# Performance work log

Hardware: AMD Instinct MI355X
Metric: run time of the kernel (lower is better)

The kernel has to match this reference:

```python
import jax, jax.numpy as jnp
import numpy as np

N, E = 50000, 400000
EMB, IN, HID, HEADS = 128, 128, 128, 3
RRELU_SLOPE = (1.0 / 8.0 + 1.0 / 3.0) / 2.0  # torch.rrelu eval-mode slope


def _gat_conv(h_in, src, dst, W, a_src, a_dst, b, concat):
    """PyG-style GATConv. h_in: [N, F_in]; src/dst: [E'] (self-loops included)."""
    n = h_in.shape[0]
    h = (h_in @ W).reshape(n, HEADS, -1)            # [N, H, C]
    e_src = jnp.sum(h * a_src, axis=-1)             # [N, H]
    e_dst = jnp.sum(h * a_dst, axis=-1)             # [N, H]
    e = jax.nn.leaky_relu(e_src[src] + e_dst[dst], 0.2)  # [E', H]
    # softmax over incoming edges of each target node
    m = jax.ops.segment_max(e, dst, num_segments=n)
    ex = jnp.exp(e - m[dst])
    denom = jax.ops.segment_sum(ex, dst, num_segments=n)
    alpha = ex / denom[dst]                          # [E', H]
    out = jax.ops.segment_sum(h[src] * alpha[:, :, None], dst, num_segments=n)  # [N,H,C]
    out = out.reshape(n, -1) if concat else out.mean(axis=1)
    return out + b


def _rrelu(x):
    return jnp.where(x >= 0, x, x * RRELU_SLOPE)


def setup_inputs() -> dict:
    key = jax.random.key(0)
    ks = jax.random.split(key, 16)
    d_in = IN + EMB

    def glorot(k, shape):
        fan = sum(shape)
        return jax.random.normal(k, shape, jnp.float32) * np.sqrt(2.0 / fan)

    return {
        "z": jax.random.normal(ks[0], (N, EMB), jnp.float32),
        "x": jax.random.normal(ks[1], (N, IN), jnp.float32),
        "ei": jax.random.randint(ks[2], (2, E), 0, N, jnp.int32),
        "W1": glorot(ks[3], (d_in, HEADS * HID)),
        "a1_src": glorot(ks[4], (HEADS, HID)),
        "a1_dst": glorot(ks[5], (HEADS, HID)),
        "b1": jnp.zeros((HID,), jnp.float32),                 # concat=False -> size C
        "W2": glorot(ks[6], (HID, HEADS * HID)),
        "a2_src": glorot(ks[7], (HEADS, HID)),
        "a2_dst": glorot(ks[8], (HEADS, HID)),
        "b2": jnp.zeros((HEADS * HID,), jnp.float32),         # concat=True -> size H*C
        "W_lin": glorot(ks[9], (HEADS * HID, 1)),
        "b_lin": jnp.zeros((1,), jnp.float32),
    }


def reference(z, x, ei, W1, a1_src, a1_dst, b1, W2, a2_src, a2_dst, b2, W_lin, b_lin):
    n = x.shape[0]
    loops = jnp.arange(n, dtype=ei.dtype)
    src = jnp.concatenate([ei[0], loops])  # PyG add_self_loops=True
    dst = jnp.concatenate([ei[1], loops])
    h = jnp.concatenate([z, x], axis=1)
    h = _rrelu(_gat_conv(h, src, dst, W1, a1_src, a1_dst, b1, concat=False))
    h = _rrelu(_gat_conv(h, src, dst, W2, a2_src, a2_dst, b2, concat=True))
    return jax.nn.sigmoid(h @ W_lin + b_lin)
```

## Files before the change

### kernel.cpp

```cpp
#include <hip/hip_runtime.h>
#include <stdint.h>

#define HEADS 3
#define HID 128
#define FDIM (HEADS * HID)

typedef __attribute__((ext_vector_type(8))) short bf16x8;
typedef __attribute__((ext_vector_type(4))) float f32x4;

__device__ __forceinline__ float lrelu(float x) { return x >= 0.f ? x : 0.2f * x; }
__device__ __forceinline__ float rrelu(float x) {
    const float SLOPE = (1.0f / 8.0f + 1.0f / 3.0f) * 0.5f;
    return x >= 0.f ? x : SLOPE * x;
}
__device__ __forceinline__ unsigned short f2bf(float f) {
    union { float f; unsigned u; } c; c.f = f;
    unsigned r = c.u + 0x7FFF + ((c.u >> 16) & 1);
    return (unsigned short)(r >> 16);
}
__device__ __forceinline__ float bflo(unsigned u) {
    union { unsigned u; float f; } c; c.u = u << 16; return c.f;
}
__device__ __forceinline__ float bfhi(unsigned u) {
    union { unsigned u; float f; } c; c.u = u & 0xffff0000u; return c.f;
}

__device__ __forceinline__ void gload_lds16(const void* g, void* l) {
    __builtin_amdgcn_global_load_lds(
        (const __attribute__((address_space(1))) void*)g,
        (__attribute__((address_space(3))) void*)l, 16, 0, 0);
}


__global__ void k_hist(const int* __restrict__ dst, int E, int* __restrict__ cnt) {
    for (int i = blockIdx.x * blockDim.x + threadIdx.x; i < E; i += gridDim.x * blockDim.x)
        atomicAdd(&cnt[dst[i]], 1);
}

#define SC_T 256
#define SC_E 8
#define SC_CHUNK (SC_T * SC_E)

__global__ __launch_bounds__(SC_T) void k_scan1(const int* __restrict__ cnt,
                                                int* __restrict__ exc,
                                                int* __restrict__ bsum, int n) {
    __shared__ int sm[SC_T];
    int b = blockIdx.x, t = threadIdx.x;
    int base = b * SC_CHUNK + t * SC_E;
    int v[SC_E];
    int s = 0;
#pragma unroll
    for (int i = 0; i < SC_E; i++) {
        int idx = base + i;
        v[i] = (idx < n) ? cnt[idx] : 0;
        s += v[i];
    }
    sm[t] = s;
    __syncthreads();
    for (int off = 1; off < SC_T; off <<= 1) {
        int x = (t >= off) ? sm[t - off] : 0;
        __syncthreads();
        sm[t] += x;
        __syncthreads();
    }
    int run = sm[t] - s;
    if (t == SC_T - 1) bsum[b] = sm[t];
#pragma unroll
    for (int i = 0; i < SC_E; i++) {
        int idx = base + i;
        if (idx < n) exc[idx] = run;
        run += v[i];
    }
}

__global__ __launch_bounds__(256) void k_scan2(const int* __restrict__ bsum,
                                               int* __restrict__ bpre, int nb) {
    __shared__ int sm[256];
    int t = threadIdx.x;
    int v = (t < nb) ? bsum[t] : 0;
    sm[t] = v;
    __syncthreads();
    for (int off = 1; off < 256; off <<= 1) {
        int x = (t >= off) ? sm[t - off] : 0;
        __syncthreads();
        sm[t] += x;
        __syncthreads();
    }
    if (t < nb) bpre[t + 1] = sm[t];
    if (t == 0) bpre[0] = 0;
}

__global__ void k_scan3(int* __restrict__ offs, const int* __restrict__ bpre,
                        int* __restrict__ cursor, int n, int nb) {
    int i = blockIdx.x * blockDim.x + threadIdx.x;
    if (i < n) {
        int o = offs[i] + bpre[i / SC_CHUNK];
        offs[i] = o;
        cursor[i] = o;
    }
    if (i == 0) offs[n] = bpre[nb];
}

__global__ void k_scatter(const int* __restrict__ src, const int* __restrict__ dst, int E,
                          int* __restrict__ cursor, int* __restrict__ ssrc,
                          int* __restrict__ sdst) {
    for (int i = blockIdx.x * blockDim.x + threadIdx.x; i < E; i += gridDim.x * blockDim.x) {
        int d = dst[i];
        int p = atomicAdd(&cursor[d], 1);
        ssrc[p] = src[i];
        sdst[p] = d;
    }
}


__global__ void k_cvt_concat(const float* __restrict__ z, const float* __restrict__ x,
                             unsigned short* __restrict__ A, int Nn, int Mpad) {
    int total = Mpad * 64;
    for (int i = blockIdx.x * blockDim.x + threadIdx.x; i < total;
         i += gridDim.x * blockDim.x) {
        int row = i >> 6;
        int c4 = (i & 63) * 4;
        float4 v = make_float4(0.f, 0.f, 0.f, 0.f);
        if (row < Nn) {
            const float* sp = (c4 < 128) ? (z + (size_t)row * 128 + c4)
                                         : (x + (size_t)row * 128 + (c4 - 128));
            v = *(const float4*)sp;
        }
        unsigned short o[4] = {f2bf(v.x), f2bf(v.y), f2bf(v.z), f2bf(v.w)};
        *(uint2*)&A[(size_t)row * 256 + c4] = *(uint2*)o;
    }
}

__global__ void k_cvt_wt(const float* __restrict__ W, unsigned short* __restrict__ WT,
                         int K, int Ncols) {
    int n = blockIdx.x;
    for (int k = threadIdx.x; k < K; k += blockDim.x)
        WT[(size_t)n * K + k] = f2bf(W[(size_t)k * Ncols + n]);
}


__global__ __launch_bounds__(256) void k_gemm_bf16(
    const unsigned short* __restrict__ A,
    const unsigned short* __restrict__ BT,
    unsigned short* __restrict__ C,
    int K, int Ncols,
    const float* __restrict__ asrc, const float* __restrict__ adst,
    float* __restrict__ es, float* __restrict__ ed, int Nnodes) {
    __shared__ __align__(16) unsigned short As[128 * 32];
    __shared__ __align__(16) unsigned short Bs[128 * 32];
    __shared__ float esP[128][2], edP[128][2];
    int tid = threadIdx.x;
    int w = tid >> 6, lane = tid & 63;
    int row0 = blockIdx.x * 128;
    int col0 = blockIdx.y * 128;
    int wr = w >> 1, wc = w & 1;

    f32x4 acc[4][4] = {};
    int frow = lane & 15;
    int fk = (lane >> 4) * 8;

    for (int k0 = 0; k0 < K; k0 += 32) {
#pragma unroll
        for (int i = 0; i < 2; i++) {
            int c = (i * 4 + w) * 64 + lane;
            gload_lds16(A + (size_t)(row0 + (c >> 2)) * K + k0 + (c & 3) * 8,
                        (char*)As + (i * 4 + w) * 1024);
        }
#pragma unroll
        for (int i = 0; i < 2; i++) {
            int c = (i * 4 + w) * 64 + lane;
            gload_lds16(BT + (size_t)(col0 + (c >> 2)) * K + k0 + (c & 3) * 8,
                        (char*)Bs + (i * 4 + w) * 1024);
        }
        asm volatile("s_waitcnt vmcnt(0)" ::: "memory");
        __syncthreads();

        bf16x8 af[4], bfr[4];
#pragma unroll
        for (int m = 0; m < 4; m++)
            af[m] = *(const bf16x8*)&As[(wr * 64 + m * 16 + frow) * 32 + fk];
#pragma unroll
        for (int n = 0; n < 4; n++)
            bfr[n] = *(const bf16x8*)&Bs[(wc * 64 + n * 16 + frow) * 32 + fk];
#pragma unroll
        for (int m = 0; m < 4; m++)
#pragma unroll
            for (int n = 0; n < 4; n++)
                acc[m][n] = __builtin_amdgcn_mfma_f32_16x16x32_bf16(af[m], bfr[n], acc[m][n], 0, 0, 0);
        __syncthreads();
    }

    int ccol = lane & 15, crow = (lane >> 4) * 4;

#pragma unroll
    for (int m = 0; m < 4; m++)
#pragma unroll
        for (int n = 0; n < 4; n++)
#pragma unroll
            for (int j = 0; j < 4; j++) {
                int r = row0 + wr * 64 + m * 16 + crow + j;
                int cc = col0 + wc * 64 + n * 16 + ccol;
                C[(size_t)r * Ncols + cc] = f2bf(acc[m][n][j]);
            }

    int head = blockIdx.y;
    float as4[4], ad4[4];
#pragma unroll
    for (int n = 0; n < 4; n++) {
        int col_sub = wc * 64 + n * 16 + ccol;
        as4[n] = asrc[head * HID + col_sub];
        ad4[n] = adst[head * HID + col_sub];
    }
#pragma unroll
    for (int m = 0; m < 4; m++)
#pragma unroll
        for (int j = 0; j < 4; j++) {
            float ps = 0.f, pd = 0.f;
#pragma unroll
            for (int n = 0; n < 4; n++) {
                float v = acc[m][n][j];
                ps = fmaf(v, as4[n], ps);
                pd = fmaf(v, ad4[n], pd);
            }
#pragma unroll
            for (int off = 1; off < 16; off <<= 1) {
                ps += __shfl_xor(ps, off);
                pd += __shfl_xor(pd, off);
            }
            if (ccol == 0) {
                int row_sub = wr * 64 + m * 16 + crow + j;
                esP[row_sub][wc] = ps;
                edP[row_sub][wc] = pd;
            }
        }
    __syncthreads();
    if (tid < 128) {
        int r = row0 + tid;
        if (r < Nnodes) {
            es[(size_t)r * 3 + head] = esP[tid][0] + esP[tid][1];
            ed[(size_t)r * 3 + head] = edP[tid][0] + edP[tid][1];
        }
    }
}


__global__ void k_edge_w(const int* __restrict__ ssrc, const int* __restrict__ sdst,
                         const float* __restrict__ es, const float* __restrict__ ed,
                         float4* __restrict__ w4, int E) {
    for (int j = blockIdx.x * blockDim.x + threadIdx.x; j < E; j += gridDim.x * blockDim.x) {
        int s = ssrc[j], d = sdst[j];
        float w0 = __expf(lrelu(es[s * 3 + 0] + ed[d * 3 + 0]));
        float w1 = __expf(lrelu(es[s * 3 + 1] + ed[d * 3 + 1]));
        float w2 = __expf(lrelu(es[s * 3 + 2] + ed[d * 3 + 2]));
        w4[j] = make_float4(w0, w1, w2, 0.f);
    }
}

__global__ void k_den(const float* __restrict__ es, const float* __restrict__ ed,
                      const int* __restrict__ offs, const float4* __restrict__ w4,
                      float4* __restrict__ wself, float4* __restrict__ invden, int Nn) {
    for (int n = blockIdx.x * blockDim.x + threadIdx.x; n < Nn; n += gridDim.x * blockDim.x) {
        float s0 = __expf(lrelu(es[n * 3 + 0] + ed[n * 3 + 0]));
        float s1 = __expf(lrelu(es[n * 3 + 1] + ed[n * 3 + 1]));
        float s2 = __expf(lrelu(es[n * 3 + 2] + ed[n * 3 + 2]));
        float d0 = s0, d1 = s1, d2 = s2;
        int j0 = offs[n], j1 = offs[n + 1];
        int j = j0;
        for (; j + 4 <= j1; j += 4) {
            float4 a = w4[j], b = w4[j + 1], c = w4[j + 2], d = w4[j + 3];
            d0 += a.x + b.x + c.x + d.x;
            d1 += a.y + b.y + c.y + d.y;
            d2 += a.z + b.z + c.z + d.z;
        }
        for (; j < j1; j++) {
            float4 w = w4[j];
            d0 += w.x; d1 += w.y; d2 += w.z;
        }
        wself[n] = make_float4(s0, s1, s2, 0.f);
        invden[n] = make_float4(1.f / d0, 1.f / d1, 1.f / d2, 0.f);
    }
}


#define EDGE_UNROLL4(body)                                                       \
    int j = j0;                                                                  \
    for (; j + 4 <= j1; j += 4) {                                                \
        int si[4]; float4 wv[4]; unsigned uu[4][3];                              \
        _Pragma("unroll") for (int e = 0; e < 4; e++) si[e] = ssrc[j + e];       \
        _Pragma("unroll") for (int e = 0; e < 4; e++) wv[e] = w4[j + e];         \
        _Pragma("unroll") for (int e = 0; e < 4; e++) {                          \
            const unsigned* rp = Hu + (size_t)si[e] * 192 + L;                   \
            uu[e][0] = rp[0]; uu[e][1] = rp[64]; uu[e][2] = rp[128];             \
        }                                                                        \
        _Pragma("unroll") for (int e = 0; e < 4; e++) { body(wv[e], uu[e]) }     \
    }                                                                            \
    for (; j < j1; j++) {                                                        \
        int s1_ = ssrc[j]; float4 w_ = w4[j];                                    \
        const unsigned* rp = Hu + (size_t)s1_ * 192 + L;                         \
        unsigned u_[3] = {rp[0], rp[64], rp[128]};                               \
        { body(w_, u_) }                                                         \
    }

#define ACC3(wv, uv)                                                             \
    a0[0] = fmaf(wv.x, bflo(uv[0]), a0[0]); a1[0] = fmaf(wv.x, bfhi(uv[0]), a1[0]); \
    a0[1] = fmaf(wv.y, bflo(uv[1]), a0[1]); a1[1] = fmaf(wv.y, bfhi(uv[1]), a1[1]); \
    a0[2] = fmaf(wv.z, bflo(uv[2]), a0[2]); a1[2] = fmaf(wv.z, bfhi(uv[2]), a1[2]);

__global__ __launch_bounds__(256) void k_agg_mean(const unsigned* __restrict__ Hu,
                                                  const float4* __restrict__ w4,
                                                  const float4* __restrict__ wself,
                                                  const float4* __restrict__ invden,
                                                  const int* __restrict__ offs,
                                                  const int* __restrict__ ssrc,
                                                  const float* __restrict__ b,
                                                  unsigned* __restrict__ out, int Nn) {
    int L = threadIdx.x & 63;
    int wstep = gridDim.x * 4;
    for (int n = blockIdx.x * 4 + (threadIdx.x >> 6); n < Nn; n += wstep) {
        float4 ws = wself[n];
        const unsigned* rp = Hu + (size_t)n * 192 + L;
        unsigned u0 = rp[0], u1 = rp[64], u2 = rp[128];
        float a0[3] = {ws.x * bflo(u0), ws.y * bflo(u1), ws.z * bflo(u2)};
        float a1[3] = {ws.x * bfhi(u0), ws.y * bfhi(u1), ws.z * bfhi(u2)};
        int j0 = offs[n], j1 = offs[n + 1];
        EDGE_UNROLL4(ACC3)
        float4 iv = invden[n];
        int c0 = 2 * L;
        float2 bb = *(const float2*)&b[c0];
        float m0 = (a0[0] * iv.x + a0[1] * iv.y + a0[2] * iv.z) * (1.f / 3.f) + bb.x;
        float m1 = (a1[0] * iv.x + a1[1] * iv.y + a1[2] * iv.z) * (1.f / 3.f) + bb.y;
        unsigned short o[2] = {f2bf(rrelu(m0)), f2bf(rrelu(m1))};
        out[(size_t)n * 64 + L] = *(unsigned*)o;
    }
}

__global__ __launch_bounds__(256) void k_agg_cat_final(const unsigned* __restrict__ Hu,
                                                       const float4* __restrict__ w4,
                                                       const float4* __restrict__ wself,
                                                       const float4* __restrict__ invden,
                                                       const int* __restrict__ offs,
                                                       const int* __restrict__ ssrc,
                                                       const float* __restrict__ b,
                                                       const float* __restrict__ Wl,
                                                       const float* __restrict__ bl,
                                                       float* __restrict__ out, int Nn) {
    int L = threadIdx.x & 63;
    int wstep = gridDim.x * 4;
    for (int n = blockIdx.x * 4 + (threadIdx.x >> 6); n < Nn; n += wstep) {
        float4 ws = wself[n];
        const unsigned* rp = Hu + (size_t)n * 192 + L;
        unsigned u0 = rp[0], u1 = rp[64], u2 = rp[128];
        float a0[3] = {ws.x * bflo(u0), ws.y * bflo(u1), ws.z * bflo(u2)};
        float a1[3] = {ws.x * bfhi(u0), ws.y * bfhi(u1), ws.z * bfhi(u2)};
        int j0 = offs[n], j1 = offs[n + 1];
        EDGE_UNROLL4(ACC3)
        float4 iv = invden[n];
        float ivv[3] = {iv.x, iv.y, iv.z};
        float p = 0.f;
#pragma unroll
        for (int k = 0; k < 3; k++) {
            int col = k * HID + 2 * L;
            float2 bb = *(const float2*)&b[col];
            float2 wl = *(const float2*)&Wl[col];
            float r0 = rrelu(a0[k] * ivv[k] + bb.x);
            float r1 = rrelu(a1[k] * ivv[k] + bb.y);
            p = fmaf(r0, wl.x, p);
            p = fmaf(r1, wl.y, p);
        }
#pragma unroll
        for (int off = 32; off > 0; off >>= 1) p += __shfl_down(p, off);
        if (L == 0) out[n] = 1.f / (1.f + __expf(-(p + bl[0])));
    }
}


extern "C" void kernel_launch(void* const* d_in, const int* in_sizes, int n_in,
                              void* d_out, int out_size, void* d_ws, size_t ws_size,
                              hipStream_t stream) {
    const float* z   = (const float*)d_in[0];
    const float* x   = (const float*)d_in[1];
    const int*   ei  = (const int*)d_in[2];
    const float* W1  = (const float*)d_in[3];
    const float* a1s = (const float*)d_in[4];
    const float* a1d = (const float*)d_in[5];
    const float* b1  = (const float*)d_in[6];
    const float* W2  = (const float*)d_in[7];
    const float* a2s = (const float*)d_in[8];
    const float* a2d = (const float*)d_in[9];
    const float* b2  = (const float*)d_in[10];
    const float* Wl  = (const float*)d_in[11];
    const float* bl  = (const float*)d_in[12];
    float* outp = (float*)d_out;

    int Nn = in_sizes[0] / 128;
    int E  = in_sizes[2] / 2;
    int Mpad = (Nn + 127) & ~127;
    int nb = (Nn + SC_CHUNK - 1) / SC_CHUNK;

    char* p = (char*)d_ws;
    auto carve = [&](size_t bytes) -> char* {
        char* r = p;
        p += (bytes + 255) & ~(size_t)255;
        return r;
    };
    int*            offs   = (int*)carve((size_t)(Nn + 1) * 4);
    int*            cursor = (int*)carve((size_t)Nn * 4);
    int*            ssrc   = (int*)carve((size_t)E * 4);
    int*            sdst   = (int*)carve((size_t)E * 4);
    int*            bsum   = (int*)carve((size_t)(nb + 1) * 4);
    int*            bpre   = (int*)carve((size_t)(nb + 1) * 4);
    float*          e1s    = (float*)carve((size_t)Nn * 3 * 4);
    float*          e1d    = (float*)carve((size_t)Nn * 3 * 4);
    float4*         w4     = (float4*)carve((size_t)E * 16);
    float4*         wself  = (float4*)carve((size_t)Nn * 16);
    float4*         invden = (float4*)carve((size_t)Nn * 16);
    unsigned short* Abf    = (unsigned short*)carve((size_t)Mpad * 256 * 2);
    unsigned short* W1T    = (unsigned short*)carve((size_t)FDIM * 256 * 2);
    unsigned short* W2T    = (unsigned short*)carve((size_t)FDIM * 128 * 2);
    unsigned short* Hbf    = (unsigned short*)carve((size_t)Mpad * FDIM * 2);
    unsigned short* H2in   = (unsigned short*)carve((size_t)Mpad * 128 * 2);

    const int* srcI = ei;
    const int* dstI = ei + E;

    hipMemsetAsync(cursor, 0, (size_t)Nn * 4, stream);
    k_hist<<<256, 256, 0, stream>>>(dstI, E, cursor);
    k_scan1<<<nb, SC_T, 0, stream>>>(cursor, offs, bsum, Nn);
    k_scan2<<<1, 256, 0, stream>>>(bsum, bpre, nb);
    k_scan3<<<(Nn + 255) / 256, 256, 0, stream>>>(offs, bpre, cursor, Nn, nb);
    k_scatter<<<256, 256, 0, stream>>>(srcI, dstI, E, cursor, ssrc, sdst);

    k_cvt_concat<<<2048, 256, 0, stream>>>(z, x, Abf, Nn, Mpad);
    k_cvt_wt<<<FDIM, 256, 0, stream>>>(W1, W1T, 256, FDIM);
    k_cvt_wt<<<FDIM, 128, 0, stream>>>(W2, W2T, 128, FDIM);
    hipMemsetAsync(H2in + (size_t)Nn * 128, 0, (size_t)(Mpad - Nn) * 128 * 2, stream);

    dim3 gg(Mpad / 128, FDIM / 128);

    k_gemm_bf16<<<gg, 256, 0, stream>>>(Abf, W1T, Hbf, 256, FDIM, a1s, a1d, e1s, e1d, Nn);
    k_edge_w<<<1024, 256, 0, stream>>>(ssrc, sdst, e1s, e1d, w4, E);
    k_den<<<(Nn + 255) / 256, 256, 0, stream>>>(e1s, e1d, offs, w4, wself, invden, Nn);
    k_agg_mean<<<2048, 256, 0, stream>>>((const unsigned*)Hbf, w4, wself, invden, offs,
                                         ssrc, b1, (unsigned*)H2in, Nn);

    k_gemm_bf16<<<gg, 256, 0, stream>>>(H2in, W2T, Hbf, 128, FDIM, a2s, a2d, e1s, e1d, Nn);
    k_edge_w<<<1024, 256, 0, stream>>>(ssrc, sdst, e1s, e1d, w4, E);
    k_den<<<(Nn + 255) / 256, 256, 0, stream>>>(e1s, e1d, offs, w4, wself, invden, Nn);
    k_agg_cat_final<<<2048, 256, 0, stream>>>((const unsigned*)Hbf, w4, wself, invden, offs,
                                              ssrc, b2, Wl, bl, outp, Nn);
}
```

Before: 266.7 us.

## Fuse fp32-to-bf16 conversion into GEMM and softmax denominator into aggregation

The first GEMM now reads z and x as fp32 directly, converting to bf16 while staging into LDS, which removes the separate concat/convert kernel and its intermediate buffer. The per-node denominator kernel is dropped: the aggregation kernels compute the self-loop weight and accumulate the softmax denominator alongside the weighted feature sum. Grid sizes for histogram and scatter are raised. In exchange, the A tile is loaded through registers instead of direct-to-LDS, which may stall the GEMM, and every lane redundantly sums the denominator.

```diff
diff --git a/kernel.cpp b/kernel.cpp
--- a/kernel.cpp
+++ b/kernel.cpp
@@ -113,24 +113,6 @@
 }
 
 
-__global__ void k_cvt_concat(const float* __restrict__ z, const float* __restrict__ x,
-                             unsigned short* __restrict__ A, int Nn, int Mpad) {
-    int total = Mpad * 64;
-    for (int i = blockIdx.x * blockDim.x + threadIdx.x; i < total;
-         i += gridDim.x * blockDim.x) {
-        int row = i >> 6;
-        int c4 = (i & 63) * 4;
-        float4 v = make_float4(0.f, 0.f, 0.f, 0.f);
-        if (row < Nn) {
-            const float* sp = (c4 < 128) ? (z + (size_t)row * 128 + c4)
-                                         : (x + (size_t)row * 128 + (c4 - 128));
-            v = *(const float4*)sp;
-        }
-        unsigned short o[4] = {f2bf(v.x), f2bf(v.y), f2bf(v.z), f2bf(v.w)};
-        *(uint2*)&A[(size_t)row * 256 + c4] = *(uint2*)o;
-    }
-}
-
 __global__ void k_cvt_wt(const float* __restrict__ W, unsigned short* __restrict__ WT,
                          int K, int Ncols) {
     int n = blockIdx.x;
@@ -139,8 +121,9 @@
 }
 
 
-__global__ __launch_bounds__(256) void k_gemm_bf16(
-    const unsigned short* __restrict__ A,
+template <bool F32A>
+__global__ __launch_bounds__(256) void k_gemm(
+    const void* __restrict__ Ap0, const void* __restrict__ Ap1, int Nn,
     const unsigned short* __restrict__ BT,
     unsigned short* __restrict__ C,
     int K, int Ncols,
@@ -160,17 +143,49 @@
     int fk = (lane >> 4) * 8;
 
     for (int k0 = 0; k0 < K; k0 += 32) {
-#pragma unroll
-        for (int i = 0; i < 2; i++) {
-            int c = (i * 4 + w) * 64 + lane;
-            gload_lds16(A + (size_t)(row0 + (c >> 2)) * K + k0 + (c & 3) * 8,
-                        (char*)As + (i * 4 + w) * 1024);
-        }
-#pragma unroll
-        for (int i = 0; i < 2; i++) {
-            int c = (i * 4 + w) * 64 + lane;
-            gload_lds16(BT + (size_t)(col0 + (c >> 2)) * K + k0 + (c & 3) * 8,
-                        (char*)Bs + (i * 4 + w) * 1024);
+        if (F32A) {
+            const float* zf = (const float*)Ap0;
+            const float* xf = (const float*)Ap1;
+            float4 va[4];
+#pragma unroll
+            for (int i = 0; i < 4; i++) {
+                int idx = i * 256 + tid;
+                int row = idx >> 3;
+                int c4 = (idx & 7) * 4;
+                int gr = row0 + row;
+                const float* sp = (k0 < 128)
+                                      ? (zf + (size_t)gr * 128 + k0 + c4)
+                                      : (xf + (size_t)gr * 128 + (k0 - 128) + c4);
+                va[i] = (gr < Nn) ? *(const float4*)sp
+                                  : make_float4(0.f, 0.f, 0.f, 0.f);
+            }
+#pragma unroll
+            for (int i = 0; i < 2; i++) {
+                int c = (i * 4 + w) * 64 + lane;
+                gload_lds16(BT + (size_t)(col0 + (c >> 2)) * K + k0 + (c & 3) * 8,
+                            (char*)Bs + (i * 4 + w) * 1024);
+            }
+#pragma unroll
+            for (int i = 0; i < 4; i++) {
+                int idx = i * 256 + tid;
+                unsigned short o[4] = {f2bf(va[i].x), f2bf(va[i].y),
+                                       f2bf(va[i].z), f2bf(va[i].w)};
+                *(uint2*)((char*)As + (size_t)idx * 8) = *(uint2*)o;
+            }
+        } else {
+            const unsigned short* A = (const unsigned short*)Ap0;
+#pragma unroll
+            for (int i = 0; i < 2; i++) {
+                int c = (i * 4 + w) * 64 + lane;
+                gload_lds16(A + (size_t)(row0 + (c >> 2)) * K + k0 + (c & 3) * 8,
+                            (char*)As + (i * 4 + w) * 1024);
+            }
+#pragma unroll
+            for (int i = 0; i < 2; i++) {
+                int c = (i * 4 + w) * 64 + lane;
+                gload_lds16(BT + (size_t)(col0 + (c >> 2)) * K + k0 + (c & 3) * 8,
+                            (char*)Bs + (i * 4 + w) * 1024);
+            }
         }
         asm volatile("s_waitcnt vmcnt(0)" ::: "memory");
         __syncthreads();
@@ -253,31 +268,6 @@
         float w1 = __expf(lrelu(es[s * 3 + 1] + ed[d * 3 + 1]));
         float w2 = __expf(lrelu(es[s * 3 + 2] + ed[d * 3 + 2]));
         w4[j] = make_float4(w0, w1, w2, 0.f);
-    }
-}
-
-__global__ void k_den(const float* __restrict__ es, const float* __restrict__ ed,
-                      const int* __restrict__ offs, const float4* __restrict__ w4,
-                      float4* __restrict__ wself, float4* __restrict__ invden, int Nn) {
-    for (int n = blockIdx.x * blockDim.x + threadIdx.x; n < Nn; n += gridDim.x * blockDim.x) {
-        float s0 = __expf(lrelu(es[n * 3 + 0] + ed[n * 3 + 0]));
-        float s1 = __expf(lrelu(es[n * 3 + 1] + ed[n * 3 + 1]));
-        float s2 = __expf(lrelu(es[n * 3 + 2] + ed[n * 3 + 2]));
-        float d0 = s0, d1 = s1, d2 = s2;
-        int j0 = offs[n], j1 = offs[n + 1];
-        int j = j0;
-        for (; j + 4 <= j1; j += 4) {
-            float4 a = w4[j], b = w4[j + 1], c = w4[j + 2], d = w4[j + 3];
-            d0 += a.x + b.x + c.x + d.x;
-            d1 += a.y + b.y + c.y + d.y;
-            d2 += a.z + b.z + c.z + d.z;
-        }
-        for (; j < j1; j++) {
-            float4 w = w4[j];
-            d0 += w.x; d1 += w.y; d2 += w.z;
-        }
-        wself[n] = make_float4(s0, s1, s2, 0.f);
-        invden[n] = make_float4(1.f / d0, 1.f / d1, 1.f / d2, 0.f);
     }
 }
 
@@ -304,12 +294,13 @@
 #define ACC3(wv, uv)                                                             \
     a0[0] = fmaf(wv.x, bflo(uv[0]), a0[0]); a1[0] = fmaf(wv.x, bfhi(uv[0]), a1[0]); \
     a0[1] = fmaf(wv.y, bflo(uv[1]), a0[1]); a1[1] = fmaf(wv.y, bfhi(uv[1]), a1[1]); \
-    a0[2] = fmaf(wv.z, bflo(uv[2]), a0[2]); a1[2] = fmaf(wv.z, bfhi(uv[2]), a1[2]);
+    a0[2] = fmaf(wv.z, bflo(uv[2]), a0[2]); a1[2] = fmaf(wv.z, bfhi(uv[2]), a1[2]); \
+    den0 += wv.x; den1 += wv.y; den2 += wv.z;
 
 __global__ __launch_bounds__(256) void k_agg_mean(const unsigned* __restrict__ Hu,
                                                   const float4* __restrict__ w4,
-                                                  const float4* __restrict__ wself,
-                                                  const float4* __restrict__ invden,
+                                                  const float* __restrict__ es,
+                                                  const float* __restrict__ ed,
                                                   const int* __restrict__ offs,
                                                   const int* __restrict__ ssrc,
                                                   const float* __restrict__ b,
@@ -317,18 +308,21 @@
     int L = threadIdx.x & 63;
     int wstep = gridDim.x * 4;
     for (int n = blockIdx.x * 4 + (threadIdx.x >> 6); n < Nn; n += wstep) {
-        float4 ws = wself[n];
+        float s0 = __expf(lrelu(es[n * 3 + 0] + ed[n * 3 + 0]));
+        float s1 = __expf(lrelu(es[n * 3 + 1] + ed[n * 3 + 1]));
+        float s2 = __expf(lrelu(es[n * 3 + 2] + ed[n * 3 + 2]));
+        float den0 = s0, den1 = s1, den2 = s2;
         const unsigned* rp = Hu + (size_t)n * 192 + L;
         unsigned u0 = rp[0], u1 = rp[64], u2 = rp[128];
-        float a0[3] = {ws.x * bflo(u0), ws.y * bflo(u1), ws.z * bflo(u2)};
-        float a1[3] = {ws.x * bfhi(u0), ws.y * bfhi(u1), ws.z * bfhi(u2)};
+        float a0[3] = {s0 * bflo(u0), s1 * bflo(u1), s2 * bflo(u2)};
+        float a1[3] = {s0 * bfhi(u0), s1 * bfhi(u1), s2 * bfhi(u2)};
         int j0 = offs[n], j1 = offs[n + 1];
         EDGE_UNROLL4(ACC3)
-        float4 iv = invden[n];
+        float iv0 = 1.f / den0, iv1 = 1.f / den1, iv2 = 1.f / den2;
         int c0 = 2 * L;
         float2 bb = *(const float2*)&b[c0];
-        float m0 = (a0[0] * iv.x + a0[1] * iv.y + a0[2] * iv.z) * (1.f / 3.f) + bb.x;
-        float m1 = (a1[0] * iv.x + a1[1] * iv.y + a1[2] * iv.z) * (1.f / 3.f) + bb.y;
+        float m0 = (a0[0] * iv0 + a0[1] * iv1 + a0[2] * iv2) * (1.f / 3.f) + bb.x;
+        float m1 = (a1[0] * iv0 + a1[1] * iv1 + a1[2] * iv2) * (1.f / 3.f) + bb.y;
         unsigned short o[2] = {f2bf(rrelu(m0)), f2bf(rrelu(m1))};
         out[(size_t)n * 64 + L] = *(unsigned*)o;
     }
@@ -336,8 +330,8 @@
 
 __global__ __launch_bounds__(256) void k_agg_cat_final(const unsigned* __restrict__ Hu,
                                                        const float4* __restrict__ w4,
-                                                       const float4* __restrict__ wself,
-                                                       const float4* __restrict__ invden,
+                                                       const float* __restrict__ es,
+                                                       const float* __restrict__ ed,
                                                        const int* __restrict__ offs,
                                                        const int* __restrict__ ssrc,
                                                        const float* __restrict__ b,
@@ -347,15 +341,17 @@
     int L = threadIdx.x & 63;
     int wstep = gridDim.x * 4;
     for (int n = blockIdx.x * 4 + (threadIdx.x >> 6); n < Nn; n += wstep) {
-        float4 ws = wself[n];
+        float s0 = __expf(lrelu(es[n * 3 + 0] + ed[n * 3 + 0]));
+        float s1 = __expf(lrelu(es[n * 3 + 1] + ed[n * 3 + 1]));
+        float s2 = __expf(lrelu(es[n * 3 + 2] + ed[n * 3 + 2]));
+        float den0 = s0, den1 = s1, den2 = s2;
         const unsigned* rp = Hu + (size_t)n * 192 + L;
         unsigned u0 = rp[0], u1 = rp[64], u2 = rp[128];
-        float a0[3] = {ws.x * bflo(u0), ws.y * bflo(u1), ws.z * bflo(u2)};
-        float a1[3] = {ws.x * bfhi(u0), ws.y * bfhi(u1), ws.z * bfhi(u2)};
+        float a0[3] = {s0 * bflo(u0), s1 * bflo(u1), s2 * bflo(u2)};
+        float a1[3] = {s0 * bfhi(u0), s1 * bfhi(u1), s2 * bfhi(u2)};
         int j0 = offs[n], j1 = offs[n + 1];
         EDGE_UNROLL4(ACC3)
-        float4 iv = invden[n];
-        float ivv[3] = {iv.x, iv.y, iv.z};
+        float ivv[3] = {1.f / den0, 1.f / den1, 1.f / den2};
         float p = 0.f;
 #pragma unroll
         for (int k = 0; k < 3; k++) {
@@ -412,9 +408,6 @@
     float*          e1s    = (float*)carve((size_t)Nn * 3 * 4);
     float*          e1d    = (float*)carve((size_t)Nn * 3 * 4);
     float4*         w4     = (float4*)carve((size_t)E * 16);
-    float4*         wself  = (float4*)carve((size_t)Nn * 16);
-    float4*         invden = (float4*)carve((size_t)Nn * 16);
-    unsigned short* Abf    = (unsigned short*)carve((size_t)Mpad * 256 * 2);
     unsigned short* W1T    = (unsigned short*)carve((size_t)FDIM * 256 * 2);
     unsigned short* W2T    = (unsigned short*)carve((size_t)FDIM * 128 * 2);
     unsigned short* Hbf    = (unsigned short*)carve((size_t)Mpad * FDIM * 2);
@@ -424,28 +417,27 @@
     const int* dstI = ei + E;
 
     hipMemsetAsync(cursor, 0, (size_t)Nn * 4, stream);
-    k_hist<<<256, 256, 0, stream>>>(dstI, E, cursor);
+    k_hist<<<1024, 256, 0, stream>>>(dstI, E, cursor);
     k_scan1<<<nb, SC_T, 0, stream>>>(cursor, offs, bsum, Nn);
     k_scan2<<<1, 256, 0, stream>>>(bsum, bpre, nb);
     k_scan3<<<(Nn + 255) / 256, 256, 0, stream>>>(offs, bpre, cursor, Nn, nb);
-    k_scatter<<<256, 256, 0, stream>>>(srcI, dstI, E, cursor, ssrc, sdst);
-
-    k_cvt_concat<<<2048, 256, 0, stream>>>(z, x, Abf, Nn, Mpad);
+    k_scatter<<<1024, 256, 0, stream>>>(srcI, dstI, E, cursor, ssrc, sdst);
+
     k_cvt_wt<<<FDIM, 256, 0, stream>>>(W1, W1T, 256, FDIM);
     k_cvt_wt<<<FDIM, 128, 0, stream>>>(W2, W2T, 128, FDIM);
     hipMemsetAsync(H2in + (size_t)Nn * 128, 0, (size_t)(Mpad - Nn) * 128 * 2, stream);
 
     dim3 gg(Mpad / 128, FDIM / 128);
 
-    k_gemm_bf16<<<gg, 256, 0, stream>>>(Abf, W1T, Hbf, 256, FDIM, a1s, a1d, e1s, e1d, Nn);
+    k_gemm<true><<<gg, 256, 0, stream>>>(z, x, Nn, W1T, Hbf, 256, FDIM,
+                                         a1s, a1d, e1s, e1d, Nn);
     k_edge_w<<<1024, 256, 0, stream>>>(ssrc, sdst, e1s, e1d, w4, E);
-    k_den<<<(Nn + 255) / 256, 256, 0, stream>>>(e1s, e1d, offs, w4, wself, invden, Nn);
-    k_agg_mean<<<2048, 256, 0, stream>>>((const unsigned*)Hbf, w4, wself, invden, offs,
+    k_agg_mean<<<2048, 256, 0, stream>>>((const unsigned*)Hbf, w4, e1s, e1d, offs,
                                          ssrc, b1, (unsigned*)H2in, Nn);
 
-    k_gemm_bf16<<<gg, 256, 0, stream>>>(H2in, W2T, Hbf, 128, FDIM, a2s, a2d, e1s, e1d, Nn);
+    k_gemm<false><<<gg, 256, 0, stream>>>(H2in, nullptr, Mpad, W2T, Hbf, 128, FDIM,
+                                          a2s, a2d, e1s, e1d, Nn);
     k_edge_w<<<1024, 256, 0, stream>>>(ssrc, sdst, e1s, e1d, w4, E);
-    k_den<<<(Nn + 255) / 256, 256, 0, stream>>>(e1s, e1d, offs, w4, wself, invden, Nn);
-    k_agg_cat_final<<<2048, 256, 0, stream>>>((const unsigned*)Hbf, w4, wself, invden, offs,
+    k_agg_cat_final<<<2048, 256, 0, stream>>>((const unsigned*)Hbf, w4, e1s, e1d, offs,
                                               ssrc, b2, Wl, bl, outp, Nn);
 }
```

After: 254.7 us. 1.05x faster.
